# Optimization experiments

Measured on AMD Instinct MI355X. Metric: run time of the kernel, lower is better.

Reference implementation:

```python
import jax, jax.numpy as jnp
import numpy as np

N_EMBD = 1024
N_HEAD = 16
HEAD_SIZE = N_EMBD // N_HEAD
EPS = 1e-5


def layer_norm(x, gamma, beta):
    mu = jnp.mean(x, axis=-1, keepdims=True)
    var = jnp.var(x, axis=-1, keepdims=True)
    return (x - mu) * jax.lax.rsqrt(var + EPS) * gamma + beta


def setup_inputs() -> dict:
    key = jax.random.key(0)
    ks = jax.random.split(key, 12)
    B, T, C, H, hs = 2, 2048, N_EMBD, N_HEAD, HEAD_SIZE
    s = lambda fan_in: 1.0 / np.sqrt(fan_in)
    return {
        "x": jax.random.normal(ks[0], (B, T, C), dtype=jnp.float32),
        "Wq": jax.random.normal(ks[1], (H, C, hs), dtype=jnp.float32) * s(C),
        "Wk": jax.random.normal(ks[2], (H, C, hs), dtype=jnp.float32) * s(C),
        "Wv": jax.random.normal(ks[3], (H, C, hs), dtype=jnp.float32) * s(C),
        "Wproj": jax.random.normal(ks[4], (C, C), dtype=jnp.float32) * s(C),
        "bproj": jax.random.normal(ks[5], (C,), dtype=jnp.float32) * 0.01,
        "g1": jnp.ones((C,), dtype=jnp.float32),
        "b1": jnp.zeros((C,), dtype=jnp.float32),
        "g2": jnp.ones((C,), dtype=jnp.float32),
        "b2": jnp.zeros((C,), dtype=jnp.float32),
        "W_ff1": jax.random.normal(ks[6], (C, 4 * C), dtype=jnp.float32) * s(C),
        "b_ff1": jax.random.normal(ks[7], (4 * C,), dtype=jnp.float32) * 0.01,
        "W_ff2": jax.random.normal(ks[8], (4 * C, C), dtype=jnp.float32) * s(4 * C),
        "b_ff2": jax.random.normal(ks[9], (C,), dtype=jnp.float32) * 0.01,
    }


def reference(x, Wq, Wk, Wv, Wproj, bproj, g1, b1, g2, b2, W_ff1, b_ff1, W_ff2, b_ff2):
    B, T, C = x.shape
    # --- LN1 + multi-head causal self-attention ---
    h = layer_norm(x, g1, b1)
    q = jnp.einsum("btc,hcd->bhtd", h, Wq)  # [B,H,T,hs]
    k = jnp.einsum("btc,hcd->bhtd", h, Wk)
    v = jnp.einsum("btc,hcd->bhtd", h, Wv)
    scale = HEAD_SIZE ** -0.5
    wei = jnp.einsum("bhtd,bhsd->bhts", q, k) * scale  # [B,H,T,T]
    mask = jnp.tril(jnp.ones((T, T), dtype=bool))
    wei = jnp.where(mask, wei, -jnp.inf)
    wei = jax.nn.softmax(wei, axis=-1)
    out = jnp.einsum("bhts,bhsd->bhtd", wei, v)  # [B,H,T,hs]
    out = out.transpose(0, 2, 1, 3).reshape(B, T, C)  # concat heads
    sa = out @ Wproj + bproj
    x = x + sa
    # --- LN2 + FFN ---
    h2 = layer_norm(x, g2, b2)
    ff = jax.nn.relu(h2 @ W_ff1 + b_ff1) @ W_ff2 + b_ff2
    return x + ff
```

## Files before the change

kernel.cpp:

```cpp
#include <hip/hip_runtime.h>
#include <hip/hip_bf16.h>

#define N_EMBD 1024
#define N_HEAD 16
#define HEADSZ 64
#define BATCH  2
#define SEQ    2048
#define ROWS   (BATCH*SEQ)

typedef __attribute__((ext_vector_type(8))) short bf16x8;
typedef __attribute__((ext_vector_type(4))) float f32x4;

__device__ __forceinline__ short f2bs(float v){
    union { __hip_bfloat16 b; short s; } u; u.b = __float2bfloat16(v); return u.s;
}
__device__ __forceinline__ short scale8th(short s){
    union { unsigned i; float f; } u; u.i = ((unsigned)(unsigned short)s) << 16;
    return f2bs(u.f * 0.125f);
}
__device__ __forceinline__ void gload16(const short* g, short* l){
    __builtin_amdgcn_global_load_lds(
        (const __attribute__((address_space(1))) unsigned int*)g,
        (__attribute__((address_space(3))) unsigned int*)l, 16, 0, 0);
}

__global__ __launch_bounds__(256) void tr_cvt(const float* __restrict__ in,
                                              short* __restrict__ out,
                                              int R, int Cc,
                                              size_t in_z, size_t out_z)
{
    __shared__ float t[32][33];
    const int tx = threadIdx.x & 31, ty = threadIdx.x >> 5;
    const int j0 = blockIdx.x * 32, i0 = blockIdx.y * 32;
    const float* ip = in + (size_t)blockIdx.z * in_z;
    short* op = out + (size_t)blockIdx.z * out_z;
#pragma unroll
    for (int p = 0; p < 4; ++p)
        t[ty + p * 8][tx] = ip[(size_t)(i0 + ty + p * 8) * Cc + j0 + tx];
    __syncthreads();
#pragma unroll
    for (int p = 0; p < 4; ++p)
        op[(size_t)(j0 + ty + p * 8) * R + i0 + tx] = f2bs(t[tx][ty + p * 8]);
}

__global__ __launch_bounds__(256) void tr3_cvt(const float* __restrict__ Wq,
                                               const float* __restrict__ Wk,
                                               const float* __restrict__ Wv,
                                               short* __restrict__ w2t)
{
    __shared__ float t[32][33];
    const int tx = threadIdx.x & 31, ty = threadIdx.x >> 5;
    const int which = blockIdx.z >> 4, head = blockIdx.z & 15;
    const int j0 = blockIdx.x * 32, i0 = blockIdx.y * 32;
    const float* ip = (which == 0 ? Wq : which == 1 ? Wk : Wv) + (size_t)head * 65536;
    short* op = w2t + (size_t)which * 1048576 + (size_t)head * 65536;
#pragma unroll
    for (int p = 0; p < 4; ++p)
        t[ty + p * 8][tx] = ip[(size_t)(i0 + ty + p * 8) * 64 + j0 + tx];
    __syncthreads();
#pragma unroll
    for (int p = 0; p < 4; ++p)
        op[(size_t)(j0 + ty + p * 8) * 1024 + i0 + tx] = f2bs(t[tx][ty + p * 8]);
}

__global__ __launch_bounds__(256) void vt_tr(const short* __restrict__ qkv,
                                             short* __restrict__ vt)
{
    __shared__ short t[64][65];
    const int tid = threadIdx.x;
    const int sr = tid >> 2, sc = (tid & 3) * 16;
    const int col0 = blockIdx.x * 64, tok0 = blockIdx.y * 64;
    const short* ip = qkv + (size_t)(tok0 + sr) * 3072 + 2048 + col0 + sc;
    bf16x8 v0 = *(const bf16x8*)ip;
    bf16x8 v1 = *(const bf16x8*)(ip + 8);
#pragma unroll
    for (int i = 0; i < 8; ++i) { t[sr][sc + i] = v0[i]; t[sr][sc + 8 + i] = v1[i]; }
    __syncthreads();
    bf16x8 a, bq;
#pragma unroll
    for (int i = 0; i < 8; ++i) { a[i] = t[sc + i][sr]; bq[i] = t[sc + 8 + i][sr]; }
    short* op = vt + (size_t)(col0 + sr) * 4096 + tok0 + sc;
    *(bf16x8*)op = a;
    *(bf16x8*)(op + 8) = bq;
}

__global__ __launch_bounds__(256) void ln_k(const float* __restrict__ x,
                                            const float* __restrict__ g,
                                            const float* __restrict__ bta,
                                            short* __restrict__ out)
{
    const int row = blockIdx.x;
    const int tid = threadIdx.x;
    const float* xr = x + (size_t)row * N_EMBD;
    float4 v = *(const float4*)(xr + tid * 4);
    float s  = v.x + v.y + v.z + v.w;
    float s2 = v.x * v.x + v.y * v.y + v.z * v.z + v.w * v.w;
#pragma unroll
    for (int off = 32; off; off >>= 1) {
        s  += __shfl_xor(s,  off, 64);
        s2 += __shfl_xor(s2, off, 64);
    }
    __shared__ float rs[4], rs2[4];
    const int wave = tid >> 6, lane = tid & 63;
    if (lane == 0) { rs[wave] = s; rs2[wave] = s2; }
    __syncthreads();
    s  = rs[0] + rs[1] + rs[2] + rs[3];
    s2 = rs2[0] + rs2[1] + rs2[2] + rs2[3];
    const float mean = s * (1.f / N_EMBD);
    const float var  = s2 * (1.f / N_EMBD) - mean * mean;
    const float rsig = rsqrtf(var + 1e-5f);
    float4 gv = *(const float4*)(g + tid * 4);
    float4 bv = *(const float4*)(bta + tid * 4);
    short4 o;
    o.x = f2bs((v.x - mean) * rsig * gv.x + bv.x);
    o.y = f2bs((v.y - mean) * rsig * gv.y + bv.y);
    o.z = f2bs((v.z - mean) * rsig * gv.z + bv.z);
    o.w = f2bs((v.w - mean) * rsig * gv.w + bv.w);
    *(short4*)(out + (size_t)row * N_EMBD + tid * 4) = o;
}

__global__ __launch_bounds__(256) void pln_fin(const float* __restrict__ p0,
                                               const float* __restrict__ p1,
                                               const float* __restrict__ bias,
                                               const float* __restrict__ x,
                                               const float* __restrict__ g,
                                               const float* __restrict__ bta,
                                               float* __restrict__ x2,
                                               short* __restrict__ h2)
{
    const int row = blockIdx.x, tid = threadIdx.x;
    const size_t base = (size_t)row * N_EMBD + tid * 4;
    float4 a  = *(const float4*)(p0 + base);
    float4 c  = *(const float4*)(p1 + base);
    float4 xx = *(const float4*)(x + base);
    float4 bb = *(const float4*)(bias + tid * 4);
    float4 v;
    v.x = a.x + c.x + xx.x + bb.x;
    v.y = a.y + c.y + xx.y + bb.y;
    v.z = a.z + c.z + xx.z + bb.z;
    v.w = a.w + c.w + xx.w + bb.w;
    *(float4*)(x2 + base) = v;
    float s  = v.x + v.y + v.z + v.w;
    float s2 = v.x * v.x + v.y * v.y + v.z * v.z + v.w * v.w;
#pragma unroll
    for (int off = 32; off; off >>= 1) {
        s  += __shfl_xor(s,  off, 64);
        s2 += __shfl_xor(s2, off, 64);
    }
    __shared__ float rs[4], rs2[4];
    const int wave = tid >> 6, lane = tid & 63;
    if (lane == 0) { rs[wave] = s; rs2[wave] = s2; }
    __syncthreads();
    s  = rs[0] + rs[1] + rs[2] + rs[3];
    s2 = rs2[0] + rs2[1] + rs2[2] + rs2[3];
    const float mean = s * (1.f / N_EMBD);
    const float var  = s2 * (1.f / N_EMBD) - mean * mean;
    const float rsig = rsqrtf(var + 1e-5f);
    float4 gv = *(const float4*)(g + tid * 4);
    float4 bv = *(const float4*)(bta + tid * 4);
    short4 o;
    o.x = f2bs((v.x - mean) * rsig * gv.x + bv.x);
    o.y = f2bs((v.y - mean) * rsig * gv.y + bv.y);
    o.z = f2bs((v.z - mean) * rsig * gv.z + bv.z);
    o.w = f2bs((v.w - mean) * rsig * gv.w + bv.w);
    *(short4*)(h2 + base) = o;
}

__global__ __launch_bounds__(256) void mfma_gemm(
    const short* __restrict__ A,
    const short* __restrict__ Bt,
    const float* __restrict__ bias,
    const float* __restrict__ resid,
    float* __restrict__ outf,
    float* __restrict__ outf2,
    short* __restrict__ outb,
    int M, int N, int K, int kz, int relu)
{
    __shared__ __align__(16) short As[2][128 * 32];
    __shared__ __align__(16) short Bs[2][128 * 32];
    const int tid  = threadIdx.x;
    const int lane = tid & 63, w = tid >> 6;
    const int quad = lane >> 4, l16 = lane & 15;
    const int row0 = blockIdx.y * 128, col0 = blockIdx.x * 128;
    const int wm = (w >> 1) * 64, wn = (w & 1) * 64;
    const int koff = blockIdx.z * kz;
    const int kend = kz ? kz : K;

    f32x4 acc[4][4];
#pragma unroll
    for (int i = 0; i < 4; ++i)
#pragma unroll
        for (int j = 0; j < 4; ++j)
            acc[i][j] = f32x4{0.f, 0.f, 0.f, 0.f};

    const int c0  = w * 128 + lane;
    const int c1  = c0 + 64;
    const int ar0 = c0 >> 2, ak0 = (((c0 & 3) ^ ((ar0 >> 1) & 3))) * 8;
    const int ar1 = c1 >> 2, ak1 = (((c1 & 3) ^ ((ar1 >> 1) & 3))) * 8;
    const short* aG0 = A  + (size_t)(row0 + ar0) * K + koff + ak0;
    const short* aG1 = A  + (size_t)(row0 + ar1) * K + koff + ak1;
    const short* bG0 = Bt + (size_t)(col0 + ar0) * K + koff + ak0;
    const short* bG1 = Bt + (size_t)(col0 + ar1) * K + koff + ak1;
    const int lofs = w * 1024;

    const int gsw = (quad ^ ((l16 >> 1) & 3)) * 8;

    gload16(aG0, As[0] + lofs);
    gload16(aG1, As[0] + lofs + 512);
    gload16(bG0, Bs[0] + lofs);
    gload16(bG1, Bs[0] + lofs + 512);
    asm volatile("s_waitcnt vmcnt(0)" ::: "memory");
    __syncthreads();

    for (int k0 = 0; k0 < kend; k0 += 32) {
        const int cur = (k0 >> 5) & 1;
        if (k0 + 32 < kend) {
            const int nxt = cur ^ 1;
            gload16(aG0 + k0 + 32, As[nxt] + lofs);
            gload16(aG1 + k0 + 32, As[nxt] + lofs + 512);
            gload16(bG0 + k0 + 32, Bs[nxt] + lofs);
            gload16(bG1 + k0 + 32, Bs[nxt] + lofs + 512);
        }

        bf16x8 af[4], bfr[4];
#pragma unroll
        for (int i = 0; i < 4; ++i)
            af[i]  = *(const bf16x8*)(As[cur] + (wm + i * 16 + l16) * 32 + gsw);
#pragma unroll
        for (int j = 0; j < 4; ++j)
            bfr[j] = *(const bf16x8*)(Bs[cur] + (wn + j * 16 + l16) * 32 + gsw);
#pragma unroll
        for (int i = 0; i < 4; ++i)
#pragma unroll
            for (int j = 0; j < 4; ++j)
                acc[i][j] = __builtin_amdgcn_mfma_f32_16x16x32_bf16(
                    af[i], bfr[j], acc[i][j], 0, 0, 0);

        asm volatile("s_waitcnt vmcnt(0)" ::: "memory");
        __syncthreads();
    }

    float* of = blockIdx.z ? outf2 : outf;
#pragma unroll
    for (int i = 0; i < 4; ++i) {
        const int rbase = row0 + wm + i * 16 + quad * 4;
#pragma unroll
        for (int j = 0; j < 4; ++j) {
            const int c = col0 + wn + j * 16 + l16;
            const float bv = bias ? bias[c] : 0.f;
#pragma unroll
            for (int r = 0; r < 4; ++r) {
                float v = acc[i][j][r] + bv;
                if (relu) v = fmaxf(v, 0.f);
                const size_t idx = (size_t)(rbase + r) * N + c;
                if (resid) v += resid[idx];
                if (outb) outb[idx] = f2bs(v);
                else      of[idx] = v;
            }
        }
    }
}

__global__ __launch_bounds__(256) void mfma_gemm64(
    const short* __restrict__ A,
    const short* __restrict__ Bt,
    float* __restrict__ outf,
    float* __restrict__ outf2,
    int K, int kz)
{
    __shared__ __align__(16) short As[2][64 * 32];
    __shared__ __align__(16) short Bs[2][128 * 32];
    const int tid  = threadIdx.x;
    const int lane = tid & 63, w = tid >> 6;
    const int quad = lane >> 4, l16 = lane & 15;
    const int lin  = (int)blockIdx.y * 8 + (int)blockIdx.x;
    const int swz  = (lin & 7) * 64 + (lin >> 3);
    const int col0 = (swz & 7) * 128;
    const int row0 = (swz >> 3) * 64;
    const int wr = w >> 1, wc = w & 1;
    const int koff = blockIdx.z * kz;

    f32x4 acc[2][4];
#pragma unroll
    for (int i = 0; i < 2; ++i)
#pragma unroll
        for (int j = 0; j < 4; ++j)
            acc[i][j] = f32x4{0.f, 0.f, 0.f, 0.f};

    const int ia  = w * 64 + lane;
    const int ar  = ia >> 2;
    const int aak = ((ia & 3) ^ ((ar >> 1) & 3)) * 8;
    const short* aG = A + (size_t)(row0 + ar) * K + koff + aak;
    const int aofs = w * 512;
    const int c0  = w * 128 + lane;
    const int c1  = c0 + 64;
    const int br0 = c0 >> 2, bk0 = ((c0 & 3) ^ ((br0 >> 1) & 3)) * 8;
    const int br1 = c1 >> 2, bk1 = ((c1 & 3) ^ ((br1 >> 1) & 3)) * 8;
    const short* bG0 = Bt + (size_t)(col0 + br0) * K + koff + bk0;
    const short* bG1 = Bt + (size_t)(col0 + br1) * K + koff + bk1;
    const int bofs = w * 1024;

    const int gsw = (quad ^ ((l16 >> 1) & 3)) * 8;

    gload16(aG, As[0] + aofs);
    gload16(bG0, Bs[0] + bofs);
    gload16(bG1, Bs[0] + bofs + 512);
    asm volatile("s_waitcnt vmcnt(0)" ::: "memory");
    __syncthreads();

    for (int k0 = 0; k0 < kz; k0 += 32) {
        const int cur = (k0 >> 5) & 1;
        if (k0 + 32 < kz) {
            const int nxt = cur ^ 1;
            gload16(aG + k0 + 32, As[nxt] + aofs);
            gload16(bG0 + k0 + 32, Bs[nxt] + bofs);
            gload16(bG1 + k0 + 32, Bs[nxt] + bofs + 512);
        }

        bf16x8 af[2], bfr[4];
#pragma unroll
        for (int i = 0; i < 2; ++i)
            af[i]  = *(const bf16x8*)(As[cur] + (wr * 32 + i * 16 + l16) * 32 + gsw);
#pragma unroll
        for (int j = 0; j < 4; ++j)
            bfr[j] = *(const bf16x8*)(Bs[cur] + (wc * 64 + j * 16 + l16) * 32 + gsw);
#pragma unroll
        for (int i = 0; i < 2; ++i)
#pragma unroll
            for (int j = 0; j < 4; ++j)
                acc[i][j] = __builtin_amdgcn_mfma_f32_16x16x32_bf16(
                    af[i], bfr[j], acc[i][j], 0, 0, 0);

        asm volatile("s_waitcnt vmcnt(0)" ::: "memory");
        __syncthreads();
    }

    float* of = blockIdx.z ? outf2 : outf;
#pragma unroll
    for (int i = 0; i < 2; ++i) {
        const int rbase = row0 + wr * 32 + i * 16 + quad * 4;
#pragma unroll
        for (int j = 0; j < 4; ++j) {
            const int c = col0 + wc * 64 + j * 16 + l16;
#pragma unroll
            for (int r = 0; r < 4; ++r)
                of[(size_t)(rbase + r) * 1024 + c] = acc[i][j][r];
        }
    }
}

__global__ __launch_bounds__(256) void ff2_fin(const float* __restrict__ p0,
                                               const float* __restrict__ bias,
                                               const float* __restrict__ x2,
                                               float* __restrict__ out)
{
    const size_t i = ((size_t)blockIdx.x * 256 + threadIdx.x) * 4;
    float4 a = *(const float4*)(p0 + i);
    float4 b = *(const float4*)(out + i);
    float4 r = *(const float4*)(x2 + i);
    float4 bb = *(const float4*)(bias + (i & 1023));
    float4 o;
    o.x = a.x + b.x + r.x + bb.x;
    o.y = a.y + b.y + r.y + bb.y;
    o.z = a.z + b.z + r.z + bb.z;
    o.w = a.w + b.w + r.w + bb.w;
    *(float4*)(out + i) = o;
}

__global__ __launch_bounds__(256) void attn_k(const short* __restrict__ qkv,
                                              const short* __restrict__ vt,
                                              short* __restrict__ att)
{
    __shared__ __align__(16) short Ks[2][64 * 64];
    __shared__ __align__(16) short Vs[2][64 * 64];
    __shared__ __align__(16) short Ps[64 * 64];
    const int tid  = threadIdx.x;
    const int lane = tid & 63, w = tid >> 6;
    const int quad = lane >> 4, l16 = lane & 15;
    const int bh = blockIdx.y, b = bh >> 4, head = bh & 15;

    const int srow = lane >> 3;
    const int sw   = ((lane & 7) ^ srow) * 8;
    const int cidx = (quad ^ (l16 & 7)) * 8;

    const int k4 = (bh >> 3) & 3;
    int qt = (k4 & 2) ? ((int)blockIdx.x ^ 16) : (int)blockIdx.x;
    if (k4 & 1) qt = 31 - qt;
    const int t0 = qt * 64;
    const int ntiles = qt + 1;

    const short* qp = qkv + (size_t)(b * SEQ + t0 + w * 16 + l16) * 3072
                      + head * 64 + quad * 8;
    bf16x8 qf0 = *(const bf16x8*)qp;
    bf16x8 qf1 = *(const bf16x8*)(qp + 32);
#pragma unroll
    for (int i = 0; i < 8; ++i) { qf0[i] = scale8th(qf0[i]); qf1[i] = scale8th(qf1[i]); }

    float mrow = -INFINITY, lrow = 0.f;
    f32x4 O[4];
#pragma unroll
    for (int jn = 0; jn < 4; ++jn) O[jn] = f32x4{0.f, 0.f, 0.f, 0.f};

    {
        const short* kg = qkv + (size_t)(b * SEQ + w * 16 + srow) * 3072
                          + 1024 + head * 64 + sw;
        const short* vg = vt + (size_t)(head * 64 + w * 16 + srow) * 4096
                          + b * SEQ + sw;
        short* kL = Ks[0] + w * 1024;
        short* vL = Vs[0] + w * 1024;
        gload16(kg, kL); gload16(kg + (size_t)8 * 3072, kL + 512);
        gload16(vg, vL); gload16(vg + (size_t)8 * 4096, vL + 512);
    }

    for (int kt = 0; kt < ntiles; ++kt) {
        const int cur = kt & 1;
        asm volatile("s_waitcnt vmcnt(0) lgkmcnt(0)\n\ts_barrier" ::: "memory");
        if (kt + 1 < ntiles) {
            const int s1 = (kt + 1) * 64;
            const short* kg = qkv + (size_t)(b * SEQ + s1 + w * 16 + srow) * 3072
                              + 1024 + head * 64 + sw;
            const short* vg = vt + (size_t)(head * 64 + w * 16 + srow) * 4096
                              + b * SEQ + s1 + sw;
            short* kL = Ks[cur ^ 1] + w * 1024;
            short* vL = Vs[cur ^ 1] + w * 1024;
            gload16(kg, kL); gload16(kg + (size_t)8 * 3072, kL + 512);
            gload16(vg, vL); gload16(vg + (size_t)8 * 4096, vL + 512);
        }

        f32x4 S[4];
        const short* Kb = Ks[cur];
#pragma unroll
        for (int jn = 0; jn < 4; ++jn) {
            S[jn] = f32x4{0.f, 0.f, 0.f, 0.f};
            const short* kp = Kb + (jn * 16 + l16) * 64;
            bf16x8 b0 = *(const bf16x8*)(kp + cidx);
            bf16x8 b1 = *(const bf16x8*)(kp + (cidx ^ 32));
            S[jn] = __builtin_amdgcn_mfma_f32_16x16x32_bf16(b0, qf0, S[jn], 0, 0, 0);
            S[jn] = __builtin_amdgcn_mfma_f32_16x16x32_bf16(b1, qf1, S[jn], 0, 0, 0);
        }

        float Sv[4][4];
        const int qrow = t0 + w * 16 + l16;
        const int s0 = kt * 64;
#pragma unroll
        for (int jn = 0; jn < 4; ++jn)
#pragma unroll
            for (int r = 0; r < 4; ++r)
                Sv[jn][r] = S[jn][r];
        if (kt == ntiles - 1) {
#pragma unroll
            for (int jn = 0; jn < 4; ++jn)
#pragma unroll
                for (int r = 0; r < 4; ++r)
                    if (s0 + jn * 16 + quad * 4 + r > qrow) Sv[jn][r] = -INFINITY;
        }
        float tmx[4];
#pragma unroll
        for (int jn = 0; jn < 4; ++jn)
            tmx[jn] = fmaxf(fmaxf(Sv[jn][0], Sv[jn][1]), fmaxf(Sv[jn][2], Sv[jn][3]));
        float pm = fmaxf(fmaxf(tmx[0], tmx[1]), fmaxf(tmx[2], tmx[3]));
        pm = fmaxf(pm, __shfl_xor(pm, 16, 64));
        pm = fmaxf(pm, __shfl_xor(pm, 32, 64));
        const float mn    = fmaxf(mrow, pm);
        const float alpha = __expf(mrow - mn);
#pragma unroll
        for (int jn = 0; jn < 4; ++jn)
#pragma unroll
            for (int r = 0; r < 4; ++r)
                Sv[jn][r] = __expf(Sv[jn][r] - mn);
        float tsm[4];
#pragma unroll
        for (int jn = 0; jn < 4; ++jn)
            tsm[jn] = (Sv[jn][0] + Sv[jn][1]) + (Sv[jn][2] + Sv[jn][3]);
        float ps = (tsm[0] + tsm[1]) + (tsm[2] + tsm[3]);
        ps += __shfl_xor(ps, 16, 64);
        ps += __shfl_xor(ps, 32, 64);
        lrow = lrow * alpha + ps;
        mrow = mn;
#pragma unroll
        for (int r = 0; r < 4; ++r) {
            const float a = __shfl(alpha, quad * 4 + r, 64);
#pragma unroll
            for (int jn = 0; jn < 4; ++jn) O[jn][r] *= a;
        }

#pragma unroll
        for (int jn = 0; jn < 4; ++jn) {
            short4 pv;
            pv.x = f2bs(Sv[jn][0]); pv.y = f2bs(Sv[jn][1]);
            pv.z = f2bs(Sv[jn][2]); pv.w = f2bs(Sv[jn][3]);
            const int prow = w * 16 + l16;
            const int pcol = jn * 16 + quad * 4;
            const int chunk = (pcol >> 3) ^ (l16 & 7);
            *(short4*)(Ps + prow * 64 + chunk * 8 + (pcol & 7)) = pv;
        }
        asm volatile("s_waitcnt lgkmcnt(0)" ::: "memory");

        const short* pp = Ps + (w * 16 + l16) * 64;
        bf16x8 pf0 = *(const bf16x8*)(pp + cidx);
        bf16x8 pf1 = *(const bf16x8*)(pp + (cidx ^ 32));
        const short* Vb = Vs[cur];
#pragma unroll
        for (int jn = 0; jn < 4; ++jn) {
            const short* vp = Vb + (jn * 16 + l16) * 64;
            bf16x8 v0 = *(const bf16x8*)(vp + cidx);
            bf16x8 v1 = *(const bf16x8*)(vp + (cidx ^ 32));
            O[jn] = __builtin_amdgcn_mfma_f32_16x16x32_bf16(pf0, v0, O[jn], 0, 0, 0);
            O[jn] = __builtin_amdgcn_mfma_f32_16x16x32_bf16(pf1, v1, O[jn], 0, 0, 0);
        }
    }

#pragma unroll
    for (int r = 0; r < 4; ++r) {
        const float lr  = __shfl(lrow, quad * 4 + r, 64);
        const float inv = 1.f / lr;
        const size_t rowoff = (size_t)(b * SEQ + t0 + w * 16 + quad * 4 + r) * N_EMBD
                              + head * 64 + l16;
#pragma unroll
        for (int jn = 0; jn < 4; ++jn)
            att[rowoff + jn * 16] = f2bs(O[jn][r] * inv);
    }
}

extern "C" void kernel_launch(void* const* d_in, const int* in_sizes, int n_in,
                              void* d_out, int out_size, void* d_ws, size_t ws_size,
                              hipStream_t stream)
{
    const float* x     = (const float*)d_in[0];
    const float* Wq    = (const float*)d_in[1];
    const float* Wk    = (const float*)d_in[2];
    const float* Wv    = (const float*)d_in[3];
    const float* Wproj = (const float*)d_in[4];
    const float* bproj = (const float*)d_in[5];
    const float* g1    = (const float*)d_in[6];
    const float* b1    = (const float*)d_in[7];
    const float* g2    = (const float*)d_in[8];
    const float* b2    = (const float*)d_in[9];
    const float* Wff1  = (const float*)d_in[10];
    const float* bff1  = (const float*)d_in[11];
    const float* Wff2  = (const float*)d_in[12];
    const float* bff2  = (const float*)d_in[13];
    float* out = (float*)d_out;

    char* ws = (char*)d_ws;
    short* w2t  = (short*)(ws + 0);
    short* wpt  = (short*)(ws + 6291456);
    short* wf1t = (short*)(ws + 8388608);
    short* wf2t = (short*)(ws + 16777216);
    short* h    = (short*)(ws + 25165824);
    short* qkv  = (short*)(ws + 33554432);
    short* vt   = (short*)(ws + 58720256);
    short* att  = (short*)(ws + 67108864);
    float* x2   = (float*)(ws + 75497472);
    short* h2   = h;
    float* p0p  = (float*)(ws + 33554432);
    float* p1p  = (float*)(ws + 50331648);
    short* ff   = qkv;
    float* p0f  = (float*)(ws + 0);

    tr3_cvt<<<dim3(2, 32, 48),  256, 0, stream>>>(Wq, Wk, Wv, w2t);
    tr_cvt<<<dim3(32, 32, 1),  256, 0, stream>>>(Wproj, wpt,  1024, 1024, 0, 0);
    tr_cvt<<<dim3(128, 32, 1), 256, 0, stream>>>(Wff1, wf1t,  1024, 4096, 0, 0);
    tr_cvt<<<dim3(32, 128, 1), 256, 0, stream>>>(Wff2, wf2t,  4096, 1024, 0, 0);

    ln_k<<<ROWS, 256, 0, stream>>>(x, g1, b1, h);
    mfma_gemm<<<dim3(3072 / 128, ROWS / 128), 256, 0, stream>>>(
        h, w2t, nullptr, nullptr, nullptr, nullptr, qkv, ROWS, 3072, N_EMBD, 0, 0);
    vt_tr<<<dim3(16, 64), 256, 0, stream>>>(qkv, vt);
    attn_k<<<dim3(32, BATCH * N_HEAD), 256, 0, stream>>>(qkv, vt, att);
    mfma_gemm64<<<dim3(8, 64, 2), 256, 0, stream>>>(att, wpt, p0p, p1p, N_EMBD, 512);
    pln_fin<<<ROWS, 256, 0, stream>>>(p0p, p1p, bproj, x, g2, b2, x2, h2);
    mfma_gemm<<<dim3(4096 / 128, ROWS / 128), 256, 0, stream>>>(
        h2, wf1t, bff1, nullptr, nullptr, nullptr, ff, ROWS, 4096, N_EMBD, 0, 1);
    mfma_gemm64<<<dim3(8, 64, 2), 256, 0, stream>>>(ff, wf2t, p0f, out, 4096, 2048);
    ff2_fin<<<ROWS * N_EMBD / 1024, 256, 0, stream>>>(p0f, bff2, x2, out);
}
```

Before: 374.8 us.

## Triple-buffer LDS in GEMM kernels with partial vmcnt waits and one barrier

Both MFMA GEMM kernels move from double to triple LDS buffering. Loads are issued two K-steps ahead, and each step waits only for the oldest batch through a partial s_waitcnt vmcnt, with a single raw s_barrier per iteration instead of a full drain plus syncthreads. This is meant to hide global-to-LDS latency behind MFMA work. It costs more LDS per block, which can reduce occupancy, and correctness relies on the compiler keeping the asm waits ordered with the LDS reads.

```diff
diff --git a/kernel.cpp b/kernel.cpp
--- a/kernel.cpp
+++ b/kernel.cpp
@@ -176,8 +176,8 @@
     short* __restrict__ outb,
     int M, int N, int K, int kz, int relu)
 {
-    __shared__ __align__(16) short As[2][128 * 32];
-    __shared__ __align__(16) short Bs[2][128 * 32];
+    __shared__ __align__(16) short As[3][128 * 32];
+    __shared__ __align__(16) short Bs[3][128 * 32];
     const int tid  = threadIdx.x;
     const int lane = tid & 63, w = tid >> 6;
     const int quad = lane >> 4, l16 = lane & 15;
@@ -185,6 +185,7 @@
     const int wm = (w >> 1) * 64, wn = (w & 1) * 64;
     const int koff = blockIdx.z * kz;
     const int kend = kz ? kz : K;
+    const int nk   = kend >> 5;
 
     f32x4 acc[4][4];
 #pragma unroll
@@ -209,18 +210,26 @@
     gload16(aG1, As[0] + lofs + 512);
     gload16(bG0, Bs[0] + lofs);
     gload16(bG1, Bs[0] + lofs + 512);
-    asm volatile("s_waitcnt vmcnt(0)" ::: "memory");
-    __syncthreads();
-
-    for (int k0 = 0; k0 < kend; k0 += 32) {
-        const int cur = (k0 >> 5) & 1;
-        if (k0 + 32 < kend) {
-            const int nxt = cur ^ 1;
-            gload16(aG0 + k0 + 32, As[nxt] + lofs);
-            gload16(aG1 + k0 + 32, As[nxt] + lofs + 512);
-            gload16(bG0 + k0 + 32, Bs[nxt] + lofs);
-            gload16(bG1 + k0 + 32, Bs[nxt] + lofs + 512);
-        }
+    if (nk > 1) {
+        gload16(aG0 + 32, As[1] + lofs);
+        gload16(aG1 + 32, As[1] + lofs + 512);
+        gload16(bG0 + 32, Bs[1] + lofs);
+        gload16(bG1 + 32, Bs[1] + lofs + 512);
+    }
+
+    for (int k = 0; k < nk; ++k) {
+        if (k + 1 < nk) asm volatile("s_waitcnt vmcnt(4)" ::: "memory");
+        else            asm volatile("s_waitcnt vmcnt(0)" ::: "memory");
+        __builtin_amdgcn_s_barrier();
+        if (k + 2 < nk) {
+            const int nb = (k + 2) % 3;
+            const int ko = (k + 2) * 32;
+            gload16(aG0 + ko, As[nb] + lofs);
+            gload16(aG1 + ko, As[nb] + lofs + 512);
+            gload16(bG0 + ko, Bs[nb] + lofs);
+            gload16(bG1 + ko, Bs[nb] + lofs + 512);
+        }
+        const int cur = k % 3;
 
         bf16x8 af[4], bfr[4];
 #pragma unroll
@@ -235,9 +244,6 @@
             for (int j = 0; j < 4; ++j)
                 acc[i][j] = __builtin_amdgcn_mfma_f32_16x16x32_bf16(
                     af[i], bfr[j], acc[i][j], 0, 0, 0);
-
-        asm volatile("s_waitcnt vmcnt(0)" ::: "memory");
-        __syncthreads();
     }
 
     float* of = blockIdx.z ? outf2 : outf;
@@ -268,8 +274,8 @@
     float* __restrict__ outf2,
     int K, int kz)
 {
-    __shared__ __align__(16) short As[2][64 * 32];
-    __shared__ __align__(16) short Bs[2][128 * 32];
+    __shared__ __align__(16) short As[3][64 * 32];
+    __shared__ __align__(16) short Bs[3][128 * 32];
     const int tid  = threadIdx.x;
     const int lane = tid & 63, w = tid >> 6;
     const int quad = lane >> 4, l16 = lane & 15;
@@ -279,6 +285,7 @@
     const int row0 = (swz >> 3) * 64;
     const int wr = w >> 1, wc = w & 1;
     const int koff = blockIdx.z * kz;
+    const int nk   = kz >> 5;
 
     f32x4 acc[2][4];
 #pragma unroll
@@ -305,17 +312,24 @@
     gload16(aG, As[0] + aofs);
     gload16(bG0, Bs[0] + bofs);
     gload16(bG1, Bs[0] + bofs + 512);
-    asm volatile("s_waitcnt vmcnt(0)" ::: "memory");
-    __syncthreads();
-
-    for (int k0 = 0; k0 < kz; k0 += 32) {
-        const int cur = (k0 >> 5) & 1;
-        if (k0 + 32 < kz) {
-            const int nxt = cur ^ 1;
-            gload16(aG + k0 + 32, As[nxt] + aofs);
-            gload16(bG0 + k0 + 32, Bs[nxt] + bofs);
-            gload16(bG1 + k0 + 32, Bs[nxt] + bofs + 512);
-        }
+    if (nk > 1) {
+        gload16(aG + 32, As[1] + aofs);
+        gload16(bG0 + 32, Bs[1] + bofs);
+        gload16(bG1 + 32, Bs[1] + bofs + 512);
+    }
+
+    for (int k = 0; k < nk; ++k) {
+        if (k + 1 < nk) asm volatile("s_waitcnt vmcnt(3)" ::: "memory");
+        else            asm volatile("s_waitcnt vmcnt(0)" ::: "memory");
+        __builtin_amdgcn_s_barrier();
+        if (k + 2 < nk) {
+            const int nb = (k + 2) % 3;
+            const int ko = (k + 2) * 32;
+            gload16(aG + ko, As[nb] + aofs);
+            gload16(bG0 + ko, Bs[nb] + bofs);
+            gload16(bG1 + ko, Bs[nb] + bofs + 512);
+        }
+        const int cur = k % 3;
 
         bf16x8 af[2], bfr[4];
 #pragma unroll
@@ -330,9 +344,6 @@
             for (int j = 0; j < 4; ++j)
                 acc[i][j] = __builtin_amdgcn_mfma_f32_16x16x32_bf16(
                     af[i], bfr[j], acc[i][j], 0, 0, 0);
-
-        asm volatile("s_waitcnt vmcnt(0)" ::: "memory");
-        __syncthreads();
     }
 
     float* of = blockIdx.z ? outf2 : outf;
```

Result: no change. 374.2 us (-0.2%).
